# Kernel tuning notes

Measured on AMD Instinct MI355X. Metric: run time of the kernel, lower is better.

The kernel has to match this reference:

```python
import jax, jax.numpy as jnp
import numpy as np

B, L, D = 2, 2048, 1024
H, QK, V = 8, 128, 128
EPS = 1e-5  # torch GroupNorm default


def setup_inputs() -> dict:
    key = jax.random.key(0)
    ks = jax.random.split(key, 6)
    sequence = jax.random.normal(ks[0], (B, L, D), jnp.float32)
    times = jnp.broadcast_to(jnp.arange(L, dtype=jnp.float32), (B, L))
    shift = D ** -0.5
    scale = 2.0 * shift
    w_q = jax.random.uniform(ks[1], (H, D, QK), jnp.float32) * scale - shift
    w_k = jax.random.uniform(ks[2], (H, D, QK), jnp.float32) * scale - shift
    w_v = jax.random.uniform(ks[3], (H, D, V), jnp.float32) * scale - shift
    out_dims = H * V
    w_g = jax.random.uniform(ks[4], (D, out_dims), jnp.float32) * scale - shift
    shift2 = out_dims ** -0.5
    scale2 = 2.0 * shift2
    w_o = jax.random.uniform(ks[5], (out_dims, out_dims), jnp.float32) * scale2 - shift2
    gn_w = jnp.ones((out_dims,), jnp.float32)
    gn_b = jnp.zeros((out_dims,), jnp.float32)
    return dict(sequence=sequence, times=times, w_q=w_q, w_k=w_k, w_v=w_v,
                w_g=w_g, w_o=w_o, gn_w=gn_w, gn_b=gn_b)


def rotate_by_i(x):
    # pairs (even, odd) -> (-odd, even), interleaved back
    x2 = x.reshape(x.shape[:-1] + (-1, 2))
    real, imag = x2[..., 0], x2[..., 1]
    return jnp.stack([-imag, real], axis=-1).reshape(x.shape)


def reference(sequence, times, w_q, w_k, w_v, w_g, w_o, gn_w, gn_b):
    gammas = 1.0 - 2.0 ** (-5.0 - jnp.arange(H, dtype=jnp.float32))            # (H,)
    thetas = 10000.0 ** (-2.0 * jnp.arange(QK // 2, dtype=jnp.float32) / QK)   # (QK/2,)

    q = jnp.einsum('bld,hdk->hblk', sequence, w_q)  # (H,B,L,QK)
    k = jnp.einsum('bld,hdk->hblk', sequence, w_k)
    v = jnp.einsum('bld,hdv->hblv', sequence, w_v)  # (H,B,L,V)

    # xPos rotor: angles interleaved-duplicated along last dim
    angles = times[..., None] * thetas              # (B,L,QK/2)
    cos = jnp.repeat(jnp.cos(angles), 2, axis=-1)   # (B,L,QK)
    sin = jnp.repeat(jnp.sin(angles), 2, axis=-1)
    q = cos * q + sin * rotate_by_i(q)
    k = cos * k - sin * rotate_by_i(k)

    # causal exponential-decay mask D[n,m] = gamma**(n-m) * (n>=m)
    mat = times[:, :, None] - times[:, None, :]     # (B,L,L)
    mask = mat >= 0
    g4 = gammas[:, None, None, None]                # (H,1,1,1)
    d = jnp.where(mask, g4 ** jnp.where(mask, mat, 0.0), 0.0)  # (H,B,L,L)

    ret = jnp.einsum('hbik,hbjk->hbij', q, k) * d   # (H,B,L,L)
    retention = jnp.einsum('hbij,hbjv->hbiv', ret, v)  # (H,B,L,V)

    # GroupNorm(num_heads, H*V): normalize each head's V channels per token
    r = jnp.transpose(retention, (1, 2, 0, 3))      # (B,L,H,V)
    mean = r.mean(-1, keepdims=True)
    var = r.var(-1, keepdims=True)
    rn = (r - mean) / jnp.sqrt(var + EPS)
    rn = rn * gn_w.reshape(H, V) + gn_b.reshape(H, V)
    rn = rn.reshape(B, L, H * V)

    g = sequence @ w_g
    gate = g * jax.nn.sigmoid(g)                    # swish
    return (gate * rn) @ w_o                        # (B,L,H*V)
```

## Files before the change

### kernel.cpp

```cpp
#include <hip/hip_runtime.h>
#include <stdint.h>

typedef unsigned short u16;
typedef unsigned int   u32;
typedef short  short8 __attribute__((ext_vector_type(8)));
typedef float  f32x4  __attribute__((ext_vector_type(4)));

#define DEV static __device__ __forceinline__

DEV float bf2f(u16 u) { u32 x = ((u32)u) << 16; float f; __builtin_memcpy(&f, &x, 4); return f; }
DEV u16 f2bf(float f) {
  u32 u; __builtin_memcpy(&u, &f, 4);
  return (u16)((u + 0x7FFFu + ((u >> 16) & 1u)) >> 16);
}
DEV bool probe_bf16(const void* times) { return *(const u32*)times == 0x3F800000u; }

DEV void gload16(const u16* g, u16* l) {
  __builtin_amdgcn_global_load_lds(
      (__attribute__((address_space(1))) void*)(u16*)g,
      (__attribute__((address_space(3))) void*)l, 16, 0, 0);
}

DEV f32x4 MFMA(short8 a, short8 b, f32x4 c) {
  return __builtin_amdgcn_mfma_f32_16x16x32_bf16(a, b, c, 0, 0, 0);
}

DEV void gemm128(const u16* Ag, const u16* Bg, int K, u16* sA, u16* sB,
                 f32x4 (&acc)[4][4]) {
  const int tid = threadIdx.x;
  const int lane = tid & 63, w = tid >> 6;
  const int wm = w >> 1, wn = w & 1;
  const int row = lane & 15, quad = lane >> 4;
  f32x4 z = {0.f, 0.f, 0.f, 0.f};
#pragma unroll
  for (int mt = 0; mt < 4; ++mt)
#pragma unroll
    for (int nt = 0; nt < 4; ++nt) acc[mt][nt] = z;

  for (int k0 = 0; k0 < K; k0 += 64) {
    __syncthreads();
#pragma unroll
    for (int i = 0; i < 4; ++i) {
      int c = (w << 2) + i;
      gload16(Ag + (size_t)(c * 8 + (lane >> 3)) * K + k0 + (lane & 7) * 8, sA + c * 544);
      gload16(Bg + (size_t)(c * 8 + (lane >> 3)) * K + k0 + (lane & 7) * 8, sB + c * 544);
    }
    __syncthreads();
#pragma unroll
    for (int kt = 0; kt < 2; ++kt) {
      short8 av[4], bv[4];
#pragma unroll
      for (int t = 0; t < 4; ++t) {
        int m = wm * 64 + t * 16 + row;
        av[t] = *(const short8*)(sA + (m >> 3) * 544 + (m & 7) * 64 + kt * 32 + quad * 8);
        int n = wn * 64 + t * 16 + row;
        bv[t] = *(const short8*)(sB + (n >> 3) * 544 + (n & 7) * 64 + kt * 32 + quad * 8);
      }
#pragma unroll
      for (int mt = 0; mt < 4; ++mt)
#pragma unroll
        for (int nt = 0; nt < 4; ++nt)
          acc[mt][nt] = MFMA(av[mt], bv[nt], acc[mt][nt]);
    }
  }
}

__global__ __launch_bounds__(256) void transpose_kernel(
    const void* wq, const void* wk, const void* wv, const void* wg,
    const void* wo, const void* times, u16* wsT) {
  __shared__ u16 T[128 * 132];
  int s = blockIdx.x, t = blockIdx.y;
  bool isbf = probe_bf16(times);
  const void* src; int ld; size_t off0;
  if (s < 8)       { src = wq; ld = 128;  off0 = (size_t)s * 131072; }
  else if (s < 16) { src = wk; ld = 128;  off0 = (size_t)(s - 8) * 131072; }
  else if (s < 24) { src = wv; ld = 128;  off0 = (size_t)(s - 16) * 131072; }
  else if (s < 32) { src = wg; ld = 1024; off0 = (size_t)(s - 24) * 128; }
  else             { src = wo; ld = 1024; off0 = (size_t)(s - 32) * 128; }
  int d0 = t * 128;
  const u16* s16 = (const u16*)src;
  const float* s32 = (const float*)src;
  for (int pass = 0; pass < 64; ++pass) {
    int idx = pass * 256 + threadIdx.x;
    int dl = idx >> 7, c = idx & 127;
    size_t goff = off0 + (size_t)(d0 + dl) * ld + c;
    T[c * 132 + dl] = isbf ? s16[goff] : f2bf(s32[goff]);
  }
  __syncthreads();
  u16* dst = wsT + (size_t)s * 131072;
  for (int pass = 0; pass < 16; ++pass) {
    int idx = pass * 256 + threadIdx.x;
    int c = idx >> 5, ch = idx & 31;
    uint2 v = *(const uint2*)&T[c * 132 + ch * 4];
    *(uint2*)&dst[(size_t)c * 1024 + d0 + ch * 4] = v;
  }
}

__global__ __launch_bounds__(256) void seq_kernel(const void* seq, const void* times, u16* dst) {
  bool isbf = probe_bf16(times);
  size_t idx = ((size_t)blockIdx.x * 256 + threadIdx.x) * 8;
  if (isbf) {
    *(uint4*)&dst[idx] = *(const uint4*)((const u16*)seq + idx);
  } else {
    const float* s = (const float*)seq;
    u32 a0 = (u32)f2bf(s[idx + 0]) | ((u32)f2bf(s[idx + 1]) << 16);
    u32 a1 = (u32)f2bf(s[idx + 2]) | ((u32)f2bf(s[idx + 3]) << 16);
    u32 a2 = (u32)f2bf(s[idx + 4]) | ((u32)f2bf(s[idx + 5]) << 16);
    u32 a3 = (u32)f2bf(s[idx + 6]) | ((u32)f2bf(s[idx + 7]) << 16);
    uint4 v; v.x = a0; v.y = a1; v.z = a2; v.w = a3;
    *(uint4*)&dst[idx] = v;
  }
}

__global__ __launch_bounds__(256, 4) void proj_kernel(
    const u16* seqb, const void* times, const u16* wsT,
    u16* qws, u16* kws, u16* vtws, u16* gatews) {
  __shared__ __align__(16) u16 smem[17408];
  u16* sA = smem;
  u16* sB = smem + 8704;
  int nb = blockIdx.x, mb = blockIdx.y;
  f32x4 acc[4][4];
  gemm128(seqb + (size_t)mb * 128 * 1024, wsT + (size_t)nb * 131072, 1024, sA, sB, acc);

  const int tid = threadIdx.x, lane = tid & 63, w = tid >> 6;
  const int wm = w >> 1, wn = w & 1, row = lane & 15, quad = lane >> 4;
  const bool isbf = probe_bf16(times);
  const u16* t16 = (const u16*)times;
  const float* t32 = (const float*)times;
  const int b = mb >> 4, l0 = (mb & 15) * 128;

  __syncthreads();

  if (nb < 16) {
    int type = nb >> 3;
    int h = nb & 7;
    float sgnk = type ? -1.f : 1.f;
#pragma unroll
    for (int mt = 0; mt < 4; ++mt) {
#pragma unroll
      for (int nt = 0; nt < 4; ++nt) {
        int c = wn * 64 + nt * 16 + row;
        float theta = exp2f(-0.2076205059304601f * (float)(c >> 1));
        float sgn = (c & 1) ? 1.f : -1.f;
#pragma unroll
        for (int r = 0; r < 4; ++r) {
          int lloc = wm * 64 + mt * 16 + quad * 4 + r;
          float v = acc[mt][nt][r];
          float pv = __shfl_xor(v, 1);
          float tv = isbf ? bf2f(t16[b * 2048 + l0 + lloc]) : t32[b * 2048 + l0 + lloc];
          float rev = theta * tv * 0.15915494309189535f;
          rev -= floorf(rev);
          float sn = __builtin_amdgcn_sinf(rev);
          float cs = __builtin_amdgcn_cosf(rev);
          float ov = cs * v + sgnk * sgn * sn * pv;
          u16 o16 = f2bf(ov);
          int other = __shfl_xor((int)o16, 1);
          if (!(lane & 1))
            *(u32*)&smem[lloc * 136 + c] = (u32)o16 | ((u32)other << 16);
        }
      }
    }
    __syncthreads();
    u16* outp = (type ? kws : qws) + (((size_t)(h * 2 + b) * 2048 + l0) << 7);
#pragma unroll
    for (int p = 0; p < 8; ++p) {
      int idx = p * 256 + tid, rr = idx >> 4, ch = idx & 15;
      *(uint4*)&outp[(size_t)rr * 128 + ch * 8] = *(const uint4*)&smem[rr * 136 + ch * 8];
    }
  } else if (nb < 24) {
    int h = nb & 7;
#pragma unroll
    for (int mt = 0; mt < 4; ++mt) {
      int lb = wm * 64 + mt * 16 + quad * 4;
#pragma unroll
      for (int nt = 0; nt < 4; ++nt) {
        int c = wn * 64 + nt * 16 + row;
        uint2 pk;
        pk.x = (u32)f2bf(acc[mt][nt][0]) | ((u32)f2bf(acc[mt][nt][1]) << 16);
        pk.y = (u32)f2bf(acc[mt][nt][2]) | ((u32)f2bf(acc[mt][nt][3]) << 16);
        *(uint2*)&smem[c * 136 + lb] = pk;
      }
    }
    __syncthreads();
    u16* outp = vtws + (size_t)(h * 2 + b) * 262144 + l0;
#pragma unroll
    for (int p = 0; p < 8; ++p) {
      int idx = p * 256 + tid, cc = idx >> 4, ch = idx & 15;
      *(uint4*)&outp[(size_t)cc * 2048 + ch * 8] = *(const uint4*)&smem[cc * 136 + ch * 8];
    }
  } else {
    int cb = nb - 24;
#pragma unroll
    for (int mt = 0; mt < 4; ++mt) {
#pragma unroll
      for (int nt = 0; nt < 4; ++nt) {
        int c = wn * 64 + nt * 16 + row;
#pragma unroll
        for (int r = 0; r < 4; ++r) {
          int lloc = wm * 64 + mt * 16 + quad * 4 + r;
          float x = acc[mt][nt][r];
          float s = x / (1.f + __expf(-x));
          u16 o16 = f2bf(s);
          int other = __shfl_xor((int)o16, 1);
          if (!(lane & 1))
            *(u32*)&smem[lloc * 136 + c] = (u32)o16 | ((u32)other << 16);
        }
      }
    }
    __syncthreads();
    u16* outp = gatews + (size_t)(mb * 128) * 1024 + (size_t)cb * 128;
#pragma unroll
    for (int p = 0; p < 8; ++p) {
      int idx = p * 256 + tid, rr = idx >> 4, ch = idx & 15;
      *(uint4*)&outp[(size_t)rr * 1024 + ch * 8] = *(const uint4*)&smem[rr * 136 + ch * 8];
    }
  }
}

__global__ __launch_bounds__(256, 2) void retention_kernel(
    const u16* qws, const u16* kws, const u16* vtws, const void* times,
    float* rws, float* rws2) {
  __shared__ __align__(16) u16 sKP[128 * 132];
  __shared__ __align__(16) u16 sV[32 * 528];
  const int bx = blockIdx.x, hb = blockIdx.y;
  int ib, jb_lo, jb_hi;
  bool second;
  if (bx < 8) { ib = bx; jb_lo = 0; jb_hi = ib + 1; second = false; }
  else {
    int idx = bx - 8;
    ib = 8 + (idx >> 1);
    int nj = ib + 1, mid = nj >> 1;
    if ((idx & 1) == 0) { jb_lo = 0;   jb_hi = mid; second = false; }
    else                { jb_lo = mid; jb_hi = nj;  second = true;  }
  }
  const int h = hb >> 1, b = hb & 1;
  const int i0 = ib * 128;
  const int tid = threadIdx.x, lane = tid & 63, w = tid >> 6;
  const int wm = w >> 1, wn = w & 1, row = lane & 15, quad = lane >> 4;
  const bool isbf = probe_bf16(times);
  const u16* t16 = (const u16*)times;
  const float* t32 = (const float*)times;
  const float gamma = 1.f - exp2f(-5.f - (float)h);
  const float l2g = log2f(gamma);

  short8 qf[4][4];
  const u16* qbase = qws + ((size_t)hb * 2048 + i0) * 128;
#pragma unroll
  for (int mt = 0; mt < 4; ++mt)
#pragma unroll
    for (int kt = 0; kt < 4; ++kt)
      qf[mt][kt] = *(const short8*)(qbase + (size_t)(wm * 64 + mt * 16 + row) * 128 + kt * 32 + quad * 8);

  float trow[4][4], rpow[4][4];
#pragma unroll
  for (int mt = 0; mt < 4; ++mt)
#pragma unroll
    for (int r = 0; r < 4; ++r) {
      int i = i0 + wm * 64 + mt * 16 + quad * 4 + r;
      float tv = isbf ? bf2f(t16[b * 2048 + i]) : t32[b * 2048 + i];
      trow[mt][r] = tv;
      rpow[mt][r] = exp2f(l2g * (tv - (float)i0));
    }

  f32x4 z = {0.f, 0.f, 0.f, 0.f};
  f32x4 oacc[4][4];
#pragma unroll
  for (int mt = 0; mt < 4; ++mt)
#pragma unroll
    for (int nt = 0; nt < 4; ++nt) oacc[mt][nt] = z;

  const u16* kbase = kws + (size_t)hb * 262144;
  const u16* vbase = vtws + (size_t)hb * 262144;

  for (int jb = jb_lo; jb < jb_hi; ++jb) {
    const int j0 = jb * 128;
    if (l2g * (float)(i0 - j0 - 258) < -57.f) continue;
    __syncthreads();
#pragma unroll
    for (int ii = 0; ii < 8; ++ii) {
      int c = w * 8 + ii;
      gload16(kbase + (size_t)(j0 + c * 4 + (lane >> 4)) * 128 + (lane & 15) * 8, sKP + c * 528);
      gload16(vbase + (size_t)(c * 4 + (lane >> 4)) * 2048 + j0 + (lane & 15) * 8, sV + c * 528);
    }
    __syncthreads();

    f32x4 p[4][4];
#pragma unroll
    for (int mt = 0; mt < 4; ++mt)
#pragma unroll
      for (int nt = 0; nt < 4; ++nt) p[mt][nt] = z;
#pragma unroll
    for (int kt = 0; kt < 4; ++kt) {
      short8 bv[4];
#pragma unroll
      for (int nt = 0; nt < 4; ++nt) {
        int jr = wn * 64 + nt * 16 + row;
        bv[nt] = *(const short8*)(sKP + (jr >> 2) * 528 + (jr & 3) * 128 + kt * 32 + quad * 8);
      }
#pragma unroll
      for (int mt = 0; mt < 4; ++mt)
#pragma unroll
        for (int nt = 0; nt < 4; ++nt)
          p[mt][nt] = MFMA(qf[mt][kt], bv[nt], p[mt][nt]);
    }

    float tcol[4], cp[4];
#pragma unroll
    for (int nt = 0; nt < 4; ++nt) {
      int j = j0 + wn * 64 + nt * 16 + row;
      float tv = isbf ? bf2f(t16[b * 2048 + j]) : t32[b * 2048 + j];
      tcol[nt] = tv;
      cp[nt] = exp2f(l2g * ((float)i0 - tv));
    }
    bool intra = (jb == ib);
    __syncthreads();
#pragma unroll
    for (int mt = 0; mt < 4; ++mt)
#pragma unroll
      for (int nt = 0; nt < 4; ++nt)
#pragma unroll
        for (int r = 0; r < 4; ++r) {
          float f = rpow[mt][r] * cp[nt];
          float val = p[mt][nt][r] * f;
          if (intra && (trow[mt][r] < tcol[nt])) val = 0.f;
          sKP[(wm * 64 + mt * 16 + quad * 4 + r) * 132 + wn * 64 + nt * 16 + row] = f2bf(val);
        }
    __syncthreads();

#pragma unroll
    for (int kt = 0; kt < 4; ++kt) {
      short8 av[4], bv[4];
#pragma unroll
      for (int mt = 0; mt < 4; ++mt)
        av[mt] = *(const short8*)(sKP + (wm * 64 + mt * 16 + row) * 132 + kt * 32 + quad * 8);
#pragma unroll
      for (int nt = 0; nt < 4; ++nt) {
        int v = wn * 64 + nt * 16 + row;
        bv[nt] = *(const short8*)(sV + (v >> 2) * 528 + (v & 3) * 128 + kt * 32 + quad * 8);
      }
#pragma unroll
      for (int mt = 0; mt < 4; ++mt)
#pragma unroll
        for (int nt = 0; nt < 4; ++nt)
          oacc[mt][nt] = MFMA(av[mt], bv[nt], oacc[mt][nt]);
    }
  }

#pragma unroll
  for (int mt = 0; mt < 4; ++mt)
#pragma unroll
    for (int nt = 0; nt < 4; ++nt)
#pragma unroll
      for (int r = 0; r < 4; ++r) {
        int i = i0 + wm * 64 + mt * 16 + quad * 4 + r;
        int v = wn * 64 + nt * 16 + row;
        if (second)
          rws2[((size_t)hb * 1024 + (i - 1024)) * 128 + v] = oacc[mt][nt][r];
        else
          rws[((size_t)hb * 2048 + i) * 128 + v] = oacc[mt][nt][r];
      }
}

__global__ __launch_bounds__(256) void norm_kernel(
    const float* rws, const float* rws2, const u16* gatews,
    const void* gnw, const void* gnb, const void* times, u16* xws) {
  int tid = threadIdx.x, lane = tid & 63, w = tid >> 6;
  int rid = blockIdx.x * 4 + w;
  int hb = rid >> 11, l = rid & 2047, h = hb >> 1, b = hb & 1;
  bool isbf = probe_bf16(times);
  float2 xv = *(const float2*)&rws[(size_t)rid * 128 + lane * 2];
  if (l >= 1024) {
    float2 x2 = *(const float2*)&rws2[((size_t)hb * 1024 + (l - 1024)) * 128 + lane * 2];
    xv.x += x2.x; xv.y += x2.y;
  }
  float s = xv.x + xv.y, ss = xv.x * xv.x + xv.y * xv.y;
#pragma unroll
  for (int o = 1; o < 64; o <<= 1) { s += __shfl_xor(s, o); ss += __shfl_xor(ss, o); }
  float mean = s * (1.f / 128.f);
  float var = fmaxf(ss * (1.f / 128.f) - mean * mean, 0.f);
  float inv = rsqrtf(var + 1e-5f);
  int c0 = h * 128 + lane * 2;
  float g0, g1, bb0, bb1;
  if (isbf) {
    g0 = bf2f(((const u16*)gnw)[c0]); g1 = bf2f(((const u16*)gnw)[c0 + 1]);
    bb0 = bf2f(((const u16*)gnb)[c0]); bb1 = bf2f(((const u16*)gnb)[c0 + 1]);
  } else {
    g0 = ((const float*)gnw)[c0]; g1 = ((const float*)gnw)[c0 + 1];
    bb0 = ((const float*)gnb)[c0]; bb1 = ((const float*)gnb)[c0 + 1];
  }
  float y0 = (xv.x - mean) * inv * g0 + bb0;
  float y1 = (xv.y - mean) * inv * g1 + bb1;
  size_t xi = ((size_t)(b * 2048 + l)) * 1024 + c0;
  float gt0 = bf2f(gatews[xi]), gt1 = bf2f(gatews[xi + 1]);
  u32 pk = (u32)f2bf(y0 * gt0) | ((u32)f2bf(y1 * gt1) << 16);
  *(u32*)&xws[xi] = pk;
}

__global__ __launch_bounds__(256, 4) void out_kernel(
    const u16* xws, const u16* wsT, const void* times, void* dout) {
  __shared__ __align__(16) u16 smem[17408];
  u16* sA = smem;
  u16* sB = smem + 8704;
  int nb = blockIdx.x, mb = blockIdx.y;
  f32x4 acc[4][4];
  gemm128(xws + (size_t)mb * 128 * 1024, wsT + (size_t)(32 + nb) * 131072, 1024, sA, sB, acc);
  const int tid = threadIdx.x, lane = tid & 63, w = tid >> 6;
  const int wm = w >> 1, wn = w & 1, row = lane & 15, quad = lane >> 4;
  bool isbf = probe_bf16(times);
  if (isbf) {
    __syncthreads();
#pragma unroll
    for (int mt = 0; mt < 4; ++mt) {
#pragma unroll
      for (int nt = 0; nt < 4; ++nt) {
        int c = wn * 64 + nt * 16 + row;
#pragma unroll
        for (int r = 0; r < 4; ++r) {
          int lloc = wm * 64 + mt * 16 + quad * 4 + r;
          u16 o16 = f2bf(acc[mt][nt][r]);
          int other = __shfl_xor((int)o16, 1);
          if (!(lane & 1))
            *(u32*)&smem[lloc * 136 + c] = (u32)o16 | ((u32)other << 16);
        }
      }
    }
    __syncthreads();
    u16* outp = (u16*)dout + (size_t)(mb * 128) * 1024 + (size_t)nb * 128;
#pragma unroll
    for (int p = 0; p < 8; ++p) {
      int idx = p * 256 + tid, rr = idx >> 4, ch = idx & 15;
      *(uint4*)&outp[(size_t)rr * 1024 + ch * 8] = *(const uint4*)&smem[rr * 136 + ch * 8];
    }
  } else {
#pragma unroll
    for (int mt = 0; mt < 4; ++mt)
#pragma unroll
      for (int nt = 0; nt < 4; ++nt)
#pragma unroll
        for (int r = 0; r < 4; ++r) {
          int i = mb * 128 + wm * 64 + mt * 16 + quad * 4 + r;
          size_t o = (size_t)i * 1024 + nb * 128 + wn * 64 + nt * 16 + row;
          ((float*)dout)[o] = acc[mt][nt][r];
        }
  }
}

extern "C" void kernel_launch(void* const* d_in, const int* in_sizes, int n_in,
                              void* d_out, int out_size, void* d_ws, size_t ws_size,
                              hipStream_t stream) {
  const void* seq   = d_in[0];
  const void* times = d_in[1];
  const void* wq = d_in[2];
  const void* wk = d_in[3];
  const void* wv = d_in[4];
  const void* wg = d_in[5];
  const void* wo = d_in[6];
  const void* gnw = d_in[7];
  const void* gnb = d_in[8];

  u16* ws = (u16*)d_ws;
  u16* wsT    = ws;
  u16* qws    = ws + 5242880;
  u16* kws    = qws + 4194304;
  u16* vtws   = kws + 4194304;
  u16* gatews = vtws + 4194304;
  float* rws  = (float*)(gatews + 4194304);
  u16* seqb   = (u16*)(rws + 4194304);
  float* rws2 = (float*)seqb;
  u16* xws    = qws;

  transpose_kernel<<<dim3(40, 8), 256, 0, stream>>>(wq, wk, wv, wg, wo, times, wsT);
  seq_kernel<<<dim3(2048), 256, 0, stream>>>(seq, times, seqb);
  proj_kernel<<<dim3(32, 32), 256, 0, stream>>>(seqb, times, wsT, qws, kws, vtws, gatews);
  retention_kernel<<<dim3(24, 16), 256, 0, stream>>>(qws, kws, vtws, times, rws, rws2);
  norm_kernel<<<dim3(8192), 256, 0, stream>>>(rws, rws2, gatews, gnw, gnb, times, xws);
  out_kernel<<<dim3(8, 32), 256, 0, stream>>>(xws, wsT, times, d_out);
}
```

Before: 287.4 us.

## Halve retention query tile to 64 rows and double the grid

The retention kernel now gives each block 64 query rows instead of 128, with four waves splitting the key/value columns. The grid goes from 24 to 48 blocks per head-batch, and blocks are ordered heaviest first so the causal triangle is better balanced across CUs. The P tile is written to LDS as packed pairs via a lane shuffle, and the masking times are loaded only for the diagonal block. Each block still loads full 128-wide K/V tiles for only 64 query rows, so K/V traffic per unit of work doubles and the skip bound is tightened to match.

```diff
diff --git a/kernel.cpp b/kernel.cpp
--- a/kernel.cpp
+++ b/kernel.cpp
@@ -220,23 +220,26 @@
 __global__ __launch_bounds__(256, 2) void retention_kernel(
     const u16* qws, const u16* kws, const u16* vtws, const void* times,
     float* rws, float* rws2) {
-  __shared__ __align__(16) u16 sKP[128 * 132];
+  __shared__ __align__(16) u16 sKP[32 * 528];
   __shared__ __align__(16) u16 sV[32 * 528];
   const int bx = blockIdx.x, hb = blockIdx.y;
-  int ib, jb_lo, jb_hi;
+  int ib64, jb_lo, jb_hi, njm1;
   bool second;
-  if (bx < 8) { ib = bx; jb_lo = 0; jb_hi = ib + 1; second = false; }
-  else {
-    int idx = bx - 8;
-    ib = 8 + (idx >> 1);
-    int nj = ib + 1, mid = nj >> 1;
-    if ((idx & 1) == 0) { jb_lo = 0;   jb_hi = mid; second = false; }
-    else                { jb_lo = mid; jb_hi = nj;  second = true;  }
+  if (bx < 32) {
+    ib64 = 31 - (bx >> 1);
+    int nj = (ib64 >> 1) + 1, mid = nj >> 1;
+    njm1 = nj - 1;
+    if ((bx & 1) == 0) { jb_lo = 0;   jb_hi = mid; second = false; }
+    else               { jb_lo = mid; jb_hi = nj;  second = true;  }
+  } else {
+    ib64 = 47 - bx;
+    njm1 = ib64 >> 1;
+    jb_lo = 0; jb_hi = njm1 + 1; second = false;
   }
   const int h = hb >> 1, b = hb & 1;
-  const int i0 = ib * 128;
-  const int tid = threadIdx.x, lane = tid & 63, w = tid >> 6;
-  const int wm = w >> 1, wn = w & 1, row = lane & 15, quad = lane >> 4;
+  const int i0 = ib64 * 64;
+  const int tid = threadIdx.x, lane = tid & 63, wn = tid >> 6;
+  const int row = lane & 15, quad = lane >> 4;
   const bool isbf = probe_bf16(times);
   const u16* t16 = (const u16*)times;
   const float* t32 = (const float*)times;
@@ -249,115 +252,128 @@
   for (int mt = 0; mt < 4; ++mt)
 #pragma unroll
     for (int kt = 0; kt < 4; ++kt)
-      qf[mt][kt] = *(const short8*)(qbase + (size_t)(wm * 64 + mt * 16 + row) * 128 + kt * 32 + quad * 8);
-
-  float trow[4][4], rpow[4][4];
+      qf[mt][kt] = *(const short8*)(qbase + (size_t)(mt * 16 + row) * 128 + kt * 32 + quad * 8);
+
+  float rpow[4][4];
 #pragma unroll
   for (int mt = 0; mt < 4; ++mt)
 #pragma unroll
     for (int r = 0; r < 4; ++r) {
-      int i = i0 + wm * 64 + mt * 16 + quad * 4 + r;
+      int i = i0 + mt * 16 + quad * 4 + r;
       float tv = isbf ? bf2f(t16[b * 2048 + i]) : t32[b * 2048 + i];
-      trow[mt][r] = tv;
       rpow[mt][r] = exp2f(l2g * (tv - (float)i0));
     }
 
   f32x4 z = {0.f, 0.f, 0.f, 0.f};
-  f32x4 oacc[4][4];
+  f32x4 oacc[4][2];
 #pragma unroll
   for (int mt = 0; mt < 4; ++mt)
 #pragma unroll
-    for (int nt = 0; nt < 4; ++nt) oacc[mt][nt] = z;
+    for (int vt = 0; vt < 2; ++vt) oacc[mt][vt] = z;
 
   const u16* kbase = kws + (size_t)hb * 262144;
   const u16* vbase = vtws + (size_t)hb * 262144;
 
   for (int jb = jb_lo; jb < jb_hi; ++jb) {
     const int j0 = jb * 128;
-    if (l2g * (float)(i0 - j0 - 258) < -57.f) continue;
+    if (l2g * (float)(i0 - j0 - 140) < -57.f) continue;
     __syncthreads();
 #pragma unroll
     for (int ii = 0; ii < 8; ++ii) {
-      int c = w * 8 + ii;
+      int c = wn * 8 + ii;
       gload16(kbase + (size_t)(j0 + c * 4 + (lane >> 4)) * 128 + (lane & 15) * 8, sKP + c * 528);
       gload16(vbase + (size_t)(c * 4 + (lane >> 4)) * 2048 + j0 + (lane & 15) * 8, sV + c * 528);
     }
     __syncthreads();
 
-    f32x4 p[4][4];
+    f32x4 p[4][2];
 #pragma unroll
     for (int mt = 0; mt < 4; ++mt)
 #pragma unroll
-      for (int nt = 0; nt < 4; ++nt) p[mt][nt] = z;
+      for (int nt = 0; nt < 2; ++nt) p[mt][nt] = z;
 #pragma unroll
     for (int kt = 0; kt < 4; ++kt) {
-      short8 bv[4];
-#pragma unroll
-      for (int nt = 0; nt < 4; ++nt) {
-        int jr = wn * 64 + nt * 16 + row;
+      short8 bv[2];
+#pragma unroll
+      for (int nt = 0; nt < 2; ++nt) {
+        int jr = wn * 32 + nt * 16 + row;
         bv[nt] = *(const short8*)(sKP + (jr >> 2) * 528 + (jr & 3) * 128 + kt * 32 + quad * 8);
       }
 #pragma unroll
       for (int mt = 0; mt < 4; ++mt)
 #pragma unroll
-        for (int nt = 0; nt < 4; ++nt)
+        for (int nt = 0; nt < 2; ++nt)
           p[mt][nt] = MFMA(qf[mt][kt], bv[nt], p[mt][nt]);
     }
 
-    float tcol[4], cp[4];
-#pragma unroll
-    for (int nt = 0; nt < 4; ++nt) {
-      int j = j0 + wn * 64 + nt * 16 + row;
+    float tcol[2], cp[2];
+#pragma unroll
+    for (int nt = 0; nt < 2; ++nt) {
+      int j = j0 + wn * 32 + nt * 16 + row;
       float tv = isbf ? bf2f(t16[b * 2048 + j]) : t32[b * 2048 + j];
       tcol[nt] = tv;
       cp[nt] = exp2f(l2g * ((float)i0 - tv));
     }
-    bool intra = (jb == ib);
+    const bool intra = (jb == njm1);
+    float trow[4][4];
+    if (intra) {
+#pragma unroll
+      for (int mt = 0; mt < 4; ++mt)
+#pragma unroll
+        for (int r = 0; r < 4; ++r) {
+          int i = i0 + mt * 16 + quad * 4 + r;
+          trow[mt][r] = isbf ? bf2f(t16[b * 2048 + i]) : t32[b * 2048 + i];
+        }
+    }
     __syncthreads();
 #pragma unroll
     for (int mt = 0; mt < 4; ++mt)
 #pragma unroll
-      for (int nt = 0; nt < 4; ++nt)
+      for (int nt = 0; nt < 2; ++nt)
 #pragma unroll
         for (int r = 0; r < 4; ++r) {
           float f = rpow[mt][r] * cp[nt];
           float val = p[mt][nt][r] * f;
           if (intra && (trow[mt][r] < tcol[nt])) val = 0.f;
-          sKP[(wm * 64 + mt * 16 + quad * 4 + r) * 132 + wn * 64 + nt * 16 + row] = f2bf(val);
+          u16 o16 = f2bf(val);
+          int other = __shfl_xor((int)o16, 1);
+          if (!(lane & 1))
+            *(u32*)&sKP[(mt * 16 + quad * 4 + r) * 132 + wn * 32 + nt * 16 + row] =
+                (u32)o16 | ((u32)other << 16);
         }
     __syncthreads();
 
 #pragma unroll
     for (int kt = 0; kt < 4; ++kt) {
-      short8 av[4], bv[4];
+      short8 av[4], bv[2];
 #pragma unroll
       for (int mt = 0; mt < 4; ++mt)
-        av[mt] = *(const short8*)(sKP + (wm * 64 + mt * 16 + row) * 132 + kt * 32 + quad * 8);
-#pragma unroll
-      for (int nt = 0; nt < 4; ++nt) {
-        int v = wn * 64 + nt * 16 + row;
-        bv[nt] = *(const short8*)(sV + (v >> 2) * 528 + (v & 3) * 128 + kt * 32 + quad * 8);
+        av[mt] = *(const short8*)(sKP + (mt * 16 + row) * 132 + kt * 32 + quad * 8);
+#pragma unroll
+      for (int vt = 0; vt < 2; ++vt) {
+        int v = wn * 32 + vt * 16 + row;
+        bv[vt] = *(const short8*)(sV + (v >> 2) * 528 + (v & 3) * 128 + kt * 32 + quad * 8);
       }
 #pragma unroll
       for (int mt = 0; mt < 4; ++mt)
 #pragma unroll
-        for (int nt = 0; nt < 4; ++nt)
-          oacc[mt][nt] = MFMA(av[mt], bv[nt], oacc[mt][nt]);
+        for (int vt = 0; vt < 2; ++vt)
+          oacc[mt][vt] = MFMA(av[mt], bv[vt], oacc[mt][vt]);
     }
   }
 
 #pragma unroll
   for (int mt = 0; mt < 4; ++mt)
 #pragma unroll
-    for (int nt = 0; nt < 4; ++nt)
+    for (int vt = 0; vt < 2; ++vt)
 #pragma unroll
       for (int r = 0; r < 4; ++r) {
-        int i = i0 + wm * 64 + mt * 16 + quad * 4 + r;
-        int v = wn * 64 + nt * 16 + row;
+        int i = i0 + mt * 16 + quad * 4 + r;
+        int v = wn * 32 + vt * 16 + row;
         if (second)
-          rws2[((size_t)hb * 1024 + (i - 1024)) * 128 + v] = oacc[mt][nt][r];
+          rws2[((size_t)hb * 1024 + (i - 1024)) * 128 + v] = oacc[mt][vt][r];
         else
-          rws[((size_t)hb * 2048 + i) * 128 + v] = oacc[mt][nt][r];
+          rws[((size_t)hb * 2048 + i) * 128 + v] = oacc[mt][vt][r];
       }
 }
 
@@ -472,7 +488,7 @@
   transpose_kernel<<<dim3(40, 8), 256, 0, stream>>>(wq, wk, wv, wg, wo, times, wsT);
   seq_kernel<<<dim3(2048), 256, 0, stream>>>(seq, times, seqb);
   proj_kernel<<<dim3(32, 32), 256, 0, stream>>>(seqb, times, wsT, qws, kws, vtws, gatews);
-  retention_kernel<<<dim3(24, 16), 256, 0, stream>>>(qws, kws, vtws, times, rws, rws2);
+  retention_kernel<<<dim3(48, 16), 256, 0, stream>>>(qws, kws, vtws, times, rws, rws2);
   norm_kernel<<<dim3(8192), 256, 0, stream>>>(rws, rws2, gatews, gnw, gnb, times, xws);
   out_kernel<<<dim3(8, 32), 256, 0, stream>>>(xws, wsT, times, d_out);
 }
```

After: 281.3 us. -2.1%, faster.
